# Kernel tuning notes

Hardware: AMD Instinct MI355X
Metric: run time of the kernel (lower is better)

The kernel has to match this reference:

```python
import jax, jax.numpy as jnp
import numpy as np

D = 128      # d_model
H = 8        # nhead
DH = D // H  # head dim
L = 3        # encoder layers
DFF = 2048   # TransformerEncoderLayer default dim_feedforward
S = 1024     # seq_len (number of VRP points)
B = 1        # batch (must be 1: original code's flat-argmax masking)


def setup_inputs() -> dict:
    key = jax.random.key(0)
    ks = jax.random.split(key, 16)
    def w(k, shape, fan_in):
        return jax.random.normal(k, shape, jnp.float32) * (1.0 / np.sqrt(fan_in))
    inp = {}
    inp['x'] = jax.random.normal(ks[0], (B, S, 2), jnp.float32)
    inp['emb_w'] = w(ks[1], (D, 2), 2); inp['emb_b'] = jnp.zeros((D,), jnp.float32)
    inp['in_proj_w'] = w(ks[2], (L, 3 * D, D), D); inp['in_proj_b'] = jnp.zeros((L, 3 * D), jnp.float32)
    inp['out_w'] = w(ks[3], (L, D, D), D); inp['out_b'] = jnp.zeros((L, D), jnp.float32)
    inp['lin1_w'] = w(ks[4], (L, DFF, D), D); inp['lin1_b'] = jnp.zeros((L, DFF), jnp.float32)
    inp['lin2_w'] = w(ks[5], (L, D, DFF), DFF); inp['lin2_b'] = jnp.zeros((L, D), jnp.float32)
    inp['ln1_g'] = jnp.ones((L, D), jnp.float32); inp['ln1_b'] = jnp.zeros((L, D), jnp.float32)
    inp['ln2_g'] = jnp.ones((L, D), jnp.float32); inp['ln2_b'] = jnp.zeros((L, D), jnp.float32)
    inp['lstm_wih'] = w(ks[6], (4 * D, D), D); inp['lstm_whh'] = w(ks[7], (4 * D, D), D)
    inp['lstm_bih'] = jnp.zeros((4 * D,), jnp.float32); inp['lstm_bhh'] = jnp.zeros((4 * D,), jnp.float32)
    inp['ptr_w1'] = w(ks[8], (D, 2 * D), 2 * D); inp['ptr_b1'] = jnp.zeros((D,), jnp.float32)
    inp['ptr_w2'] = w(ks[9], (1, D), D); inp['ptr_b2'] = jnp.zeros((1,), jnp.float32)
    return inp


def _ln(x, g, b, eps=1e-5):
    mu = jnp.mean(x, axis=-1, keepdims=True)
    v = jnp.mean((x - mu) ** 2, axis=-1, keepdims=True)
    return (x - mu) * jax.lax.rsqrt(v + eps) * g + b


def reference(x, emb_w, emb_b, in_proj_w, in_proj_b, out_w, out_b,
              lin1_w, lin1_b, lin2_w, lin2_b, ln1_g, ln1_b, ln2_g, ln2_b,
              lstm_wih, lstm_whh, lstm_bih, lstm_bhh,
              ptr_w1, ptr_b1, ptr_w2, ptr_b2):
    Bz, Sz, _ = x.shape
    # embedding + seq-first layout (torch: permute(1,0,2)) -> [S, B, D]
    xe = (x @ emb_w.T + emb_b).transpose(1, 0, 2)
    scale = 1.0 / np.sqrt(DH)
    # post-norm TransformerEncoder, eval mode (dropout off)
    for l in range(L):
        qkv = xe @ in_proj_w[l].T + in_proj_b[l]                 # [S,B,3D]
        q, k, v = jnp.split(qkv, 3, axis=-1)
        q = q.reshape(Sz, Bz, H, DH)
        k = k.reshape(Sz, Bz, H, DH)
        v = v.reshape(Sz, Bz, H, DH)
        att = jax.nn.softmax(jnp.einsum('qbhd,kbhd->bhqk', q, k) * scale, axis=-1)
        ao = jnp.einsum('bhqk,kbhd->qbhd', att, v).reshape(Sz, Bz, D)
        ao = ao @ out_w[l].T + out_b[l]
        x1 = _ln(xe + ao, ln1_g[l], ln1_b[l])
        ff = jax.nn.relu(x1 @ lin1_w[l].T + lin1_b[l]) @ lin2_w[l].T + lin2_b[l]
        xe = _ln(x1 + ff, ln2_g[l], ln2_b[l])
    encoded = xe                                                  # [S,B,D]

    def lstm_step(inp, h, c):
        g = inp @ lstm_wih.T + lstm_bih + h @ lstm_whh.T + lstm_bhh
        i, f, gc, o = jnp.split(g, 4, axis=-1)                    # torch gate order i,f,g,o
        c = jax.nn.sigmoid(f) * c + jax.nn.sigmoid(i) * jnp.tanh(gc)
        h = jax.nn.sigmoid(o) * jnp.tanh(c)
        return h, c

    def step(carry, _):
        h, c, dec, mask = carry
        h, c = lstm_step(dec, h, c)                               # [B,D]
        pi = jnp.concatenate([encoded, jnp.broadcast_to(h[None], (Sz, Bz, D))], axis=-1)
        logits = (jax.nn.relu(pi @ ptr_w1.T + ptr_b1) @ ptr_w2.T + ptr_b2)[..., 0]  # [S,B]
        logits = jnp.where(mask, -jnp.inf, logits)
        # torch: mask[out.argmax()] = True -> flat argmax == row index when B==1
        mask = mask.at[jnp.argmax(logits)].set(True)
        idx = jnp.argmax(logits, axis=0)                          # [B]
        dec = jnp.take(encoded, idx, axis=0)[0]                   # torch encoded[idx] -> [1,1,D] for B=1
        return (h, c, dec, mask), logits

    carry0 = (jnp.zeros((Bz, D), x.dtype), jnp.zeros((Bz, D), x.dtype),
              encoded[0], jnp.zeros((Sz, Bz), dtype=bool))
    _, logits_all = jax.lax.scan(step, carry0, None, length=Sz - 1)
    return logits_all                                             # [S-1, S, B]
```

## Files before the change

### kernel.cpp

```cpp
#include <hip/hip_runtime.h>
#include <hip/hip_runtime_api.h>
#include <math.h>

typedef unsigned long long ull;

#define F4(p) (*(const float4*)(p))

#define NEG_BIG (-3.0e38f)

__global__ void k_embed(const float* __restrict__ x, const float* __restrict__ ew,
                        const float* __restrict__ eb, float* __restrict__ xe) {
  int i = blockIdx.x * blockDim.x + threadIdx.x;
  int s = i >> 7, d = i & 127;
  xe[i] = fmaf(x[2 * s], ew[2 * d], fmaf(x[2 * s + 1], ew[2 * d + 1], eb[d]));
}

__global__ __launch_bounds__(256) void k_gemm64(
    const float* __restrict__ A, int lda,
    const float* __restrict__ W, int ldw,
    const float* __restrict__ bias, const float* __restrict__ bias2,
    const float* __restrict__ R, float* __restrict__ C,
    int N, int K, int relu) {
  __shared__ __align__(16) float At[32][72];
  __shared__ __align__(16) float Wt[32][72];
  const int t = threadIdx.x;
  const int bm = blockIdx.x, bn = blockIdx.y;
  const int lr = t >> 3;
  const int lk = (t & 7) * 4;
  const int ty = t >> 4, tx = t & 15;
  float acc[4][4];
#pragma unroll
  for (int i = 0; i < 4; ++i)
#pragma unroll
    for (int j = 0; j < 4; ++j) acc[i][j] = 0.f;

  const float* Ab = A + (bm * 64) * lda;
  const float* Wb = W + (bn * 64) * ldw;
  for (int kt = 0; kt < K; kt += 32) {
    float4 a0 = F4(Ab + lr * lda + kt + lk);
    float4 a1 = F4(Ab + (lr + 32) * lda + kt + lk);
    float4 w0 = F4(Wb + lr * ldw + kt + lk);
    float4 w1 = F4(Wb + (lr + 32) * ldw + kt + lk);
    __syncthreads();
    At[lk + 0][lr] = a0.x; At[lk + 1][lr] = a0.y; At[lk + 2][lr] = a0.z; At[lk + 3][lr] = a0.w;
    At[lk + 0][lr + 32] = a1.x; At[lk + 1][lr + 32] = a1.y; At[lk + 2][lr + 32] = a1.z; At[lk + 3][lr + 32] = a1.w;
    Wt[lk + 0][lr] = w0.x; Wt[lk + 1][lr] = w0.y; Wt[lk + 2][lr] = w0.z; Wt[lk + 3][lr] = w0.w;
    Wt[lk + 0][lr + 32] = w1.x; Wt[lk + 1][lr + 32] = w1.y; Wt[lk + 2][lr + 32] = w1.z; Wt[lk + 3][lr + 32] = w1.w;
    __syncthreads();
#pragma unroll
    for (int kk = 0; kk < 32; ++kk) {
      float4 av = F4(&At[kk][4 * ty]);
      float4 wv = F4(&Wt[kk][4 * tx]);
      acc[0][0] = fmaf(av.x, wv.x, acc[0][0]);
      acc[0][1] = fmaf(av.x, wv.y, acc[0][1]);
      acc[0][2] = fmaf(av.x, wv.z, acc[0][2]);
      acc[0][3] = fmaf(av.x, wv.w, acc[0][3]);
      acc[1][0] = fmaf(av.y, wv.x, acc[1][0]);
      acc[1][1] = fmaf(av.y, wv.y, acc[1][1]);
      acc[1][2] = fmaf(av.y, wv.z, acc[1][2]);
      acc[1][3] = fmaf(av.y, wv.w, acc[1][3]);
      acc[2][0] = fmaf(av.z, wv.x, acc[2][0]);
      acc[2][1] = fmaf(av.z, wv.y, acc[2][1]);
      acc[2][2] = fmaf(av.z, wv.z, acc[2][2]);
      acc[2][3] = fmaf(av.z, wv.w, acc[2][3]);
      acc[3][0] = fmaf(av.w, wv.x, acc[3][0]);
      acc[3][1] = fmaf(av.w, wv.y, acc[3][1]);
      acc[3][2] = fmaf(av.w, wv.z, acc[3][2]);
      acc[3][3] = fmaf(av.w, wv.w, acc[3][3]);
    }
  }
#pragma unroll
  for (int i = 0; i < 4; ++i) {
#pragma unroll
    for (int j = 0; j < 4; ++j) {
      int row = bm * 64 + 4 * ty + i, col = bn * 64 + 4 * tx + j;
      float v = acc[i][j];
      if (bias) v += bias[col];
      if (bias2) v += bias2[col];
      if (R) v += R[row * N + col];
      if (relu) v = fmaxf(v, 0.f);
      C[row * N + col] = v;
    }
  }
}

__global__ __launch_bounds__(256) void k_gemm32(
    const float* __restrict__ A, int lda,
    const float* __restrict__ W, int ldw,
    const float* __restrict__ bias, const float* __restrict__ bias2,
    const float* __restrict__ R, float* __restrict__ C,
    int N, int K, int relu) {
  __shared__ __align__(16) float As[32][33];
  __shared__ __align__(16) float Ws[32][33];
  const int t = threadIdx.x;
  const int bm = blockIdx.x, bn = blockIdx.y;
  const int lr = t >> 3;
  const int lk = (t & 7) * 4;
  const int ty = t >> 4, tx = t & 15;
  float a00 = 0.f, a01 = 0.f, a10 = 0.f, a11 = 0.f;
  const float* Ab = A + (bm * 32) * lda;
  const float* Wb = W + (bn * 32) * ldw;
  for (int kt = 0; kt < K; kt += 32) {
    float4 av = F4(Ab + lr * lda + kt + lk);
    float4 wv = F4(Wb + lr * ldw + kt + lk);
    __syncthreads();
    As[lr][lk + 0] = av.x; As[lr][lk + 1] = av.y; As[lr][lk + 2] = av.z; As[lr][lk + 3] = av.w;
    Ws[lr][lk + 0] = wv.x; Ws[lr][lk + 1] = wv.y; Ws[lr][lk + 2] = wv.z; Ws[lr][lk + 3] = wv.w;
    __syncthreads();
#pragma unroll
    for (int kk = 0; kk < 32; ++kk) {
      float x0 = As[2 * ty][kk], x1 = As[2 * ty + 1][kk];
      float y0 = Ws[2 * tx][kk], y1 = Ws[2 * tx + 1][kk];
      a00 = fmaf(x0, y0, a00);
      a01 = fmaf(x0, y1, a01);
      a10 = fmaf(x1, y0, a10);
      a11 = fmaf(x1, y1, a11);
    }
  }
  float accs[2][2] = {{a00, a01}, {a10, a11}};
#pragma unroll
  for (int i = 0; i < 2; ++i) {
#pragma unroll
    for (int j = 0; j < 2; ++j) {
      int row = bm * 32 + 2 * ty + i, col = bn * 32 + 2 * tx + j;
      float v = accs[i][j];
      if (bias) v += bias[col];
      if (bias2) v += bias2[col];
      if (R) v += R[row * N + col];
      if (relu) v = fmaxf(v, 0.f);
      C[row * N + col] = v;
    }
  }
}

__global__ void k_ln(const float* __restrict__ in, const float* __restrict__ g,
                     const float* __restrict__ bln, float* __restrict__ out) {
  int r = blockIdx.x, t = threadIdx.x;
  float a = in[r * 128 + t], c = in[r * 128 + 64 + t];
  float sum = a + c;
#pragma unroll
  for (int off = 32; off >= 1; off >>= 1) sum += __shfl_xor(sum, off);
  float mu = sum * 0.0078125f;
  float da = a - mu, dc = c - mu;
  float v = fmaf(da, da, dc * dc);
#pragma unroll
  for (int off = 32; off >= 1; off >>= 1) v += __shfl_xor(v, off);
  float rs = rsqrtf(fmaf(v, 0.0078125f, 1e-5f));
  out[r * 128 + t] = fmaf(da * rs, g[t], bln[t]);
  out[r * 128 + 64 + t] = fmaf(dc * rs, g[64 + t], bln[64 + t]);
}

__global__ __launch_bounds__(512) void k_attn(const float* __restrict__ qkv,
                                              float* __restrict__ ao) {
  __shared__ __align__(16) float Kt[16][128];
  __shared__ __align__(16) float Vt[16][128];
  const int h = blockIdx.x, qt = blockIdx.y;
  const int t = threadIdx.x;
  const int ql = t >> 4, part = t & 15;
  const int qrow = qt * 32 + ql;
  float qv[16];
#pragma unroll
  for (int i4 = 0; i4 < 4; ++i4) {
    float4 f = F4(qkv + qrow * 384 + h * 16 + 4 * i4);
    qv[4 * i4 + 0] = f.x; qv[4 * i4 + 1] = f.y; qv[4 * i4 + 2] = f.z; qv[4 * i4 + 3] = f.w;
  }
  float m = -INFINITY, l = 0.f;
  float o[16];
#pragma unroll
  for (int i = 0; i < 16; ++i) o[i] = 0.f;

  const int jl = t >> 2, c4 = (t & 3) * 4;
  for (int jt = 0; jt < 8; ++jt) {
    __syncthreads();
    float4 kf = F4(qkv + (jt * 128 + jl) * 384 + 128 + h * 16 + c4);
    float4 vf = F4(qkv + (jt * 128 + jl) * 384 + 256 + h * 16 + c4);
    Kt[c4 + 0][jl] = kf.x; Kt[c4 + 1][jl] = kf.y; Kt[c4 + 2][jl] = kf.z; Kt[c4 + 3][jl] = kf.w;
    Vt[c4 + 0][jl] = vf.x; Vt[c4 + 1][jl] = vf.y; Vt[c4 + 2][jl] = vf.z; Vt[c4 + 3][jl] = vf.w;
    __syncthreads();
    for (int jj = 0; jj < 8; ++jj) {
      int j2 = jj * 16 + part;
      float sc = 0.f;
#pragma unroll
      for (int i = 0; i < 16; ++i) sc = fmaf(qv[i], Kt[i][j2], sc);
      sc *= 0.25f;
      float mn = fmaxf(m, sc);
      float corr = __expf(m - mn);
      float p = __expf(sc - mn);
      l = fmaf(l, corr, p);
#pragma unroll
      for (int i = 0; i < 16; ++i) o[i] = fmaf(o[i], corr, p * Vt[i][j2]);
      m = mn;
    }
  }
#pragma unroll
  for (int off = 1; off < 16; off <<= 1) {
    float m2 = __shfl_xor(m, off), l2 = __shfl_xor(l, off);
    float M = fmaxf(m, m2);
    float c1 = __expf(m - M), c2 = __expf(m2 - M);
    l = l * c1 + l2 * c2;
#pragma unroll
    for (int i = 0; i < 16; ++i) {
      float o2 = __shfl_xor(o[i], off);
      o[i] = o[i] * c1 + o2 * c2;
    }
    m = M;
  }
  if (part == 0) {
    float inv = 1.f / l;
#pragma unroll
    for (int i = 0; i < 16; ++i) ao[qrow * 128 + h * 16 + i] = o[i] * inv;
  }
}

__global__ void k_esum(const float* __restrict__ E1, const float* __restrict__ w2,
                       const float* __restrict__ b2, float* __restrict__ Es) {
  int s = blockIdx.x, t = threadIdx.x;
  float p = E1[s * 128 + t] * w2[t] + E1[s * 128 + 64 + t] * w2[64 + t];
#pragma unroll
  for (int off = 32; off >= 1; off >>= 1) p += __shfl_xor(p, off);
  if (t == 0) Es[s] = fmaf(0.5f, p, b2[0]);
}

__global__ void k_zero(ull* slots) {
  int i = blockIdx.x * blockDim.x + threadIdx.x;
  if (i < 4092) slots[i] = 0ULL;
}

#define DEC_LDS_FLOATS 35352
#define DEC_LDS_BYTES (DEC_LDS_FLOATS * 4)

__global__ __launch_bounds__(1024) void k_decoder(
    const float* __restrict__ E1, const float* __restrict__ Esum2,
    const float* __restrict__ G, const float* __restrict__ Whh,
    const float* __restrict__ PW1, const float* __restrict__ w2,
    ull* __restrict__ slots, float* __restrict__ out) {
  extern __shared__ float lds[];
  float* e1t = lds;
  float* hbuf = lds + 32896;
  float* gbuf = hbuf + 128;
  float* ginb = gbuf + 512;
  float* hpb = ginb + 512;
  float* w2hb = hpb + 128;
  float* accb = w2hb + 128;
  float* redv = accb + 1024;
  int* redi = (int*)(redv + 4);
  ull* keyb = (ull*)(redv + 8);
  float* hsumb = (float*)(keyb + 4);

  const int t = threadIdx.x, b = blockIdx.x;
  const int s = t & 255, q = t >> 8;
  const int r = t >> 1, half = t & 1;
  const int dd = t >> 3, oct = t & 7;

  float whh_reg[64];
#pragma unroll
  for (int kk = 0; kk < 16; ++kk) {
    float4 f = F4(Whh + r * 128 + half * 64 + kk * 4);
    whh_reg[4 * kk + 0] = f.x; whh_reg[4 * kk + 1] = f.y;
    whh_reg[4 * kk + 2] = f.z; whh_reg[4 * kk + 3] = f.w;
  }
  float w1_reg[16];
#pragma unroll
  for (int kk = 0; kk < 4; ++kk) {
    float4 f = F4(PW1 + dd * 256 + 128 + oct * 16 + kk * 4);
    w1_reg[4 * kk + 0] = f.x; w1_reg[4 * kk + 1] = f.y;
    w1_reg[4 * kk + 2] = f.z; w1_reg[4 * kk + 3] = f.w;
  }
  float esum_reg = 0.f, maskf = 0.f;
  if (q == 0) esum_reg = Esum2[b * 256 + s];
  float cval = 0.f;
  float curg = 0.f;
  if (t < 512) curg = G[t];

#pragma unroll
  for (int it = 0; it < 8; ++it) {
    int idx = t + it * 1024;
    int srow = idx >> 5, c4 = (idx & 31) * 4;
    float4 f = F4(E1 + (b * 256 + srow) * 128 + c4);
    e1t[(c4 + 0) * 257 + srow] = f.x;
    e1t[(c4 + 1) * 257 + srow] = f.y;
    e1t[(c4 + 2) * 257 + srow] = f.z;
    e1t[(c4 + 3) * 257 + srow] = f.w;
  }
  if (t < 128) {
    w2hb[t] = 0.5f * w2[t];
    hbuf[t] = 0.f;
  }
  __syncthreads();

#pragma unroll 1
  for (int st = 0; st < 1023; ++st) {
    float p = 0.f;
#pragma unroll
    for (int kk = 0; kk < 16; ++kk) {
      float4 hv = F4(hbuf + half * 64 + kk * 4);
      p = fmaf(whh_reg[4 * kk + 0], hv.x, p);
      p = fmaf(whh_reg[4 * kk + 1], hv.y, p);
      p = fmaf(whh_reg[4 * kk + 2], hv.z, p);
      p = fmaf(whh_reg[4 * kk + 3], hv.w, p);
    }
    p += __shfl_xor(p, 1);
    if (half == 0) gbuf[r] = p;
    if (t < 512) ginb[t] = curg;
    __syncthreads();

    if (t < 128) {
      float gi = gbuf[t] + ginb[t];
      float gf = gbuf[128 + t] + ginb[128 + t];
      float gg = gbuf[256 + t] + ginb[256 + t];
      float go = gbuf[384 + t] + ginb[384 + t];
      float si = 1.f / (1.f + expf(-gi));
      float sf = 1.f / (1.f + expf(-gf));
      float so = 1.f / (1.f + expf(-go));
      float tg = tanhf(gg);
      cval = fmaf(sf, cval, si * tg);
      hbuf[t] = so * tanhf(cval);
    }
    __syncthreads();

    float p2 = 0.f;
#pragma unroll
    for (int kk = 0; kk < 4; ++kk) {
      float4 hv = F4(hbuf + oct * 16 + kk * 4);
      p2 = fmaf(w1_reg[4 * kk + 0], hv.x, p2);
      p2 = fmaf(w1_reg[4 * kk + 1], hv.y, p2);
      p2 = fmaf(w1_reg[4 * kk + 2], hv.z, p2);
      p2 = fmaf(w1_reg[4 * kk + 3], hv.w, p2);
    }
    p2 += __shfl_xor(p2, 1);
    p2 += __shfl_xor(p2, 2);
    p2 += __shfl_xor(p2, 4);
    if (oct == 0) hpb[dd] = p2;
    __syncthreads();

    if (t < 64) {
      float hs = hpb[t] * w2hb[t] + hpb[64 + t] * w2hb[64 + t];
#pragma unroll
      for (int off = 32; off >= 1; off >>= 1) hs += __shfl_xor(hs, off);
      if (t == 0) hsumb[0] = hs;
    }
    float acc = 0.f;
    {
      const float* ebase = e1t + (q * 32) * 257 + s;
      const float* hpq = hpb + q * 32;
      const float* w2q = w2hb + q * 32;
#pragma unroll
      for (int c = 0; c < 8; ++c) {
        float4 hp4 = F4(hpq + c * 4);
        float4 w4 = F4(w2q + c * 4);
        float e0 = ebase[(c * 4 + 0) * 257];
        float e1v = ebase[(c * 4 + 1) * 257];
        float e2 = ebase[(c * 4 + 2) * 257];
        float e3 = ebase[(c * 4 + 3) * 257];
        float y0 = e0 + hp4.x, y1 = e1v + hp4.y, y2 = e2 + hp4.z, y3 = e3 + hp4.w;
        acc = fmaf(w4.x, fabsf(y0), acc);
        acc = fmaf(w4.y, fabsf(y1), acc);
        acc = fmaf(w4.z, fabsf(y2), acc);
        acc = fmaf(w4.w, fabsf(y3), acc);
      }
    }
    accb[q * 256 + s] = acc;
    __syncthreads();

    if (t < 256) {
      float a = accb[t] + accb[256 + t] + accb[512 + t] + accb[768 + t];
      float logit = esum_reg + hsumb[0] + a;
      if (maskf != 0.f) logit = NEG_BIG;
      out[st * 1024 + b * 256 + t] = logit;
      float bv = logit;
      int bi = t;
#pragma unroll
      for (int off = 32; off >= 1; off >>= 1) {
        float ov = __shfl_down(bv, off);
        int oi = __shfl_down(bi, off);
        if (ov > bv || (ov == bv && oi < bi)) { bv = ov; bi = oi; }
      }
      if ((t & 63) == 0) { redv[t >> 6] = bv; redi[t >> 6] = bi; }
    }
    __syncthreads();

    if (t == 0) {
      float bv = redv[0];
      int bi = redi[0];
      for (int w = 1; w < 4; ++w) {
        float ov = redv[w];
        int oi = redi[w];
        if (ov > bv || (ov == bv && oi < bi)) { bv = ov; bi = oi; }
      }
      unsigned u = __float_as_uint(bv);
      u = (u & 0x80000000u) ? ~u : (u | 0x80000000u);
      ull key = (1ULL << 60) | ((ull)u << 12) | (ull)(1023 - (b * 256 + bi));
      __hip_atomic_store(&slots[st * 4 + b], key, __ATOMIC_RELEASE,
                         __HIP_MEMORY_SCOPE_AGENT);
    }
    if (t < 4) {
      ull k;
      do {
        k = __hip_atomic_load(&slots[st * 4 + t], __ATOMIC_ACQUIRE,
                              __HIP_MEMORY_SCOPE_AGENT);
      } while (k == 0ULL);
      keyb[t] = k;
    }
    __syncthreads();

    ull bk = keyb[0];
    if (keyb[1] > bk) bk = keyb[1];
    if (keyb[2] > bk) bk = keyb[2];
    if (keyb[3] > bk) bk = keyb[3];
    int gidx = 1023 - (int)(bk & 0xFFFull);
    if (q == 0 && (b * 256 + s) == gidx) maskf = 1.f;
    if (t < 512) curg = G[gidx * 512 + t];
  }
}

extern "C" void kernel_launch(void* const* d_in, const int* in_sizes, int n_in,
                              void* d_out, int out_size, void* d_ws, size_t ws_size,
                              hipStream_t stream) {
  (void)in_sizes; (void)n_in; (void)out_size; (void)ws_size;
  const float* x = (const float*)d_in[0];
  const float* emb_w = (const float*)d_in[1];
  const float* emb_b = (const float*)d_in[2];
  const float* in_proj_w = (const float*)d_in[3];
  const float* in_proj_b = (const float*)d_in[4];
  const float* out_w = (const float*)d_in[5];
  const float* out_b = (const float*)d_in[6];
  const float* lin1_w = (const float*)d_in[7];
  const float* lin1_b = (const float*)d_in[8];
  const float* lin2_w = (const float*)d_in[9];
  const float* lin2_b = (const float*)d_in[10];
  const float* ln1_g = (const float*)d_in[11];
  const float* ln1_b = (const float*)d_in[12];
  const float* ln2_g = (const float*)d_in[13];
  const float* ln2_b = (const float*)d_in[14];
  const float* lstm_wih = (const float*)d_in[15];
  const float* lstm_whh = (const float*)d_in[16];
  const float* lstm_bih = (const float*)d_in[17];
  const float* lstm_bhh = (const float*)d_in[18];
  const float* ptr_w1 = (const float*)d_in[19];
  const float* ptr_b1 = (const float*)d_in[20];
  const float* ptr_w2 = (const float*)d_in[21];
  const float* ptr_b2 = (const float*)d_in[22];

  float* ws = (float*)d_ws;
  float* xe = ws + 0;
  float* x1 = ws + 131072;
  float* tmp = ws + 262144;
  float* ao = ws + 393216;
  float* qkv = ws + 524288;
  float* ff = ws + 917504;
  float* Gb = ws + 3014656;
  float* E1b = ws + 3538944;
  float* Esb = ws + 3670016;
  ull* slots = (ull*)(ws + 3671040);

  hipFuncSetAttribute((const void*)k_decoder,
                      hipFuncAttributeMaxDynamicSharedMemorySize, DEC_LDS_BYTES);

  k_embed<<<256, 512, 0, stream>>>(x, emb_w, emb_b, xe);
  for (int l = 0; l < 3; ++l) {
    k_gemm64<<<dim3(16, 6), 256, 0, stream>>>(xe, 128, in_proj_w + l * 384 * 128, 128,
        in_proj_b + l * 384, nullptr, nullptr, qkv, 384, 128, 0);
    k_attn<<<dim3(8, 32), 512, 0, stream>>>(qkv, ao);
    k_gemm32<<<dim3(32, 4), 256, 0, stream>>>(ao, 128, out_w + l * 128 * 128, 128,
        out_b + l * 128, nullptr, xe, tmp, 128, 128, 0);
    k_ln<<<1024, 64, 0, stream>>>(tmp, ln1_g + l * 128, ln1_b + l * 128, x1);
    k_gemm64<<<dim3(16, 32), 256, 0, stream>>>(x1, 128, lin1_w + l * 2048 * 128, 128,
        lin1_b + l * 2048, nullptr, nullptr, ff, 2048, 128, 1);
    k_gemm32<<<dim3(32, 4), 256, 0, stream>>>(ff, 2048, lin2_w + l * 128 * 2048, 2048,
        lin2_b + l * 128, nullptr, x1, tmp, 128, 2048, 0);
    k_ln<<<1024, 64, 0, stream>>>(tmp, ln2_g + l * 128, ln2_b + l * 128, xe);
  }
  k_gemm64<<<dim3(16, 8), 256, 0, stream>>>(xe, 128, lstm_wih, 128, lstm_bih, lstm_bhh,
      nullptr, Gb, 512, 128, 0);
  k_gemm32<<<dim3(32, 4), 256, 0, stream>>>(xe, 128, ptr_w1, 256, ptr_b1, nullptr,
      nullptr, E1b, 128, 128, 0);
  k_esum<<<1024, 64, 0, stream>>>(E1b, ptr_w2, ptr_b2, Esb);
  k_zero<<<16, 256, 0, stream>>>(slots);
  k_decoder<<<4, 1024, DEC_LDS_BYTES, stream>>>(E1b, Esb, Gb, lstm_whh, ptr_w1, ptr_w2,
      slots, (float*)d_out);
}
```

Measured before the change: 7.476 ms.

## Collapse decoder argmax and cross-block exchange into one wavefront with atomic max

Moves the per-step argmax into a single wavefront that builds packed value/index keys and reduces them with shuffles. Each block then publishes its key with an atomic fetch_max and polls all four slots inside the same wave, which removes one block-wide barrier and the serial thread-0 merge. Logit stores go to other waves in parallel, and the next step's input-gate row is fetched by wave 0 straight into LDS. Relaxed atomics replace release/acquire, which relies on the loop's barriers and atomics for correct ordering. Adds a launch bound hint and a larger LDS allocation.

Result: faster. 7.013 ms (-6.2%).

```diff
diff --git a/kernel.cpp b/kernel.cpp
--- a/kernel.cpp
+++ b/kernel.cpp
@@ -226,10 +226,10 @@
   if (i < 4092) slots[i] = 0ULL;
 }
 
-#define DEC_LDS_FLOATS 35352
+#define DEC_LDS_FLOATS 35840
 #define DEC_LDS_BYTES (DEC_LDS_FLOATS * 4)
 
-__global__ __launch_bounds__(1024) void k_decoder(
+__global__ __launch_bounds__(1024, 4) void k_decoder(
     const float* __restrict__ E1, const float* __restrict__ Esum2,
     const float* __restrict__ G, const float* __restrict__ Whh,
     const float* __restrict__ PW1, const float* __restrict__ w2,
@@ -241,16 +241,15 @@
   float* ginb = gbuf + 512;
   float* hpb = ginb + 512;
   float* w2hb = hpb + 128;
-  float* accb = w2hb + 128;
-  float* redv = accb + 1024;
-  int* redi = (int*)(redv + 4);
-  ull* keyb = (ull*)(redv + 8);
-  float* hsumb = (float*)(keyb + 4);
+  float* esumb = w2hb + 128;
+  float* maskb = esumb + 256;
+  float* accb = maskb + 256;
 
   const int t = threadIdx.x, b = blockIdx.x;
   const int s = t & 255, q = t >> 8;
   const int r = t >> 1, half = t & 1;
   const int dd = t >> 3, oct = t & 7;
+  const int L = t & 63, wv = t >> 6;
 
   float whh_reg[64];
 #pragma unroll
@@ -266,11 +265,7 @@
     w1_reg[4 * kk + 0] = f.x; w1_reg[4 * kk + 1] = f.y;
     w1_reg[4 * kk + 2] = f.z; w1_reg[4 * kk + 3] = f.w;
   }
-  float esum_reg = 0.f, maskf = 0.f;
-  if (q == 0) esum_reg = Esum2[b * 256 + s];
   float cval = 0.f;
-  float curg = 0.f;
-  if (t < 512) curg = G[t];
 
 #pragma unroll
   for (int it = 0; it < 8; ++it) {
@@ -282,11 +277,12 @@
     e1t[(c4 + 2) * 257 + srow] = f.z;
     e1t[(c4 + 3) * 257 + srow] = f.w;
   }
-  if (t < 128) {
-    w2hb[t] = 0.5f * w2[t];
-    hbuf[t] = 0.f;
-  }
+  if (t < 128) { w2hb[t] = 0.5f * w2[t]; hbuf[t] = 0.f; }
+  if (t < 256) { esumb[t] = Esum2[b * 256 + t]; maskb[t] = 0.f; }
+  if (t < 512) ginb[t] = G[t];
   __syncthreads();
+
+  int gidx = 0;
 
 #pragma unroll 1
   for (int st = 0; st < 1023; ++st) {
@@ -301,7 +297,6 @@
     }
     p += __shfl_xor(p, 1);
     if (half == 0) gbuf[r] = p;
-    if (t < 512) ginb[t] = curg;
     __syncthreads();
 
     if (t < 128) {
@@ -333,12 +328,6 @@
     if (oct == 0) hpb[dd] = p2;
     __syncthreads();
 
-    if (t < 64) {
-      float hs = hpb[t] * w2hb[t] + hpb[64 + t] * w2hb[64 + t];
-#pragma unroll
-      for (int off = 32; off >= 1; off >>= 1) hs += __shfl_xor(hs, off);
-      if (t == 0) hsumb[0] = hs;
-    }
     float acc = 0.f;
     {
       const float* ebase = e1t + (q * 32) * 257 + s;
@@ -362,54 +351,66 @@
     accb[q * 256 + s] = acc;
     __syncthreads();
 
-    if (t < 256) {
-      float a = accb[t] + accb[256 + t] + accb[512 + t] + accb[768 + t];
-      float logit = esum_reg + hsumb[0] + a;
-      if (maskf != 0.f) logit = NEG_BIG;
-      out[st * 1024 + b * 256 + t] = logit;
-      float bv = logit;
-      int bi = t;
-#pragma unroll
-      for (int off = 32; off >= 1; off >>= 1) {
-        float ov = __shfl_down(bv, off);
-        int oi = __shfl_down(bi, off);
-        if (ov > bv || (ov == bv && oi < bi)) { bv = ov; bi = oi; }
-      }
-      if ((t & 63) == 0) { redv[t >> 6] = bv; redi[t >> 6] = bi; }
-    }
-    __syncthreads();
-
-    if (t == 0) {
-      float bv = redv[0];
-      int bi = redi[0];
-      for (int w = 1; w < 4; ++w) {
-        float ov = redv[w];
-        int oi = redi[w];
-        if (ov > bv || (ov == bv && oi < bi)) { bv = ov; bi = oi; }
-      }
-      unsigned u = __float_as_uint(bv);
-      u = (u & 0x80000000u) ? ~u : (u | 0x80000000u);
-      ull key = (1ULL << 60) | ((ull)u << 12) | (ull)(1023 - (b * 256 + bi));
-      __hip_atomic_store(&slots[st * 4 + b], key, __ATOMIC_RELEASE,
-                         __HIP_MEMORY_SCOPE_AGENT);
-    }
-    if (t < 4) {
-      ull k;
-      do {
-        k = __hip_atomic_load(&slots[st * 4 + t], __ATOMIC_ACQUIRE,
-                              __HIP_MEMORY_SCOPE_AGENT);
-      } while (k == 0ULL);
-      keyb[t] = k;
-    }
-    __syncthreads();
-
-    ull bk = keyb[0];
-    if (keyb[1] > bk) bk = keyb[1];
-    if (keyb[2] > bk) bk = keyb[2];
-    if (keyb[3] > bk) bk = keyb[3];
-    int gidx = 1023 - (int)(bk & 0xFFFull);
-    if (q == 0 && (b * 256 + s) == gidx) maskf = 1.f;
-    if (t < 512) curg = G[gidx * 512 + t];
+    if (wv == 0) {
+      float hs = hpb[L] * w2hb[L] + hpb[64 + L] * w2hb[64 + L];
+#pragma unroll
+      for (int off = 32; off >= 1; off >>= 1) hs += __shfl_xor(hs, off);
+      ull bk = 0;
+#pragma unroll
+      for (int j = 0; j < 4; ++j) {
+        int rr = L + 64 * j;
+        float a = (accb[rr] + accb[256 + rr]) + (accb[512 + rr] + accb[768 + rr]);
+        float lg = esumb[rr] + hs + a;
+        if (maskb[rr] != 0.f) lg = NEG_BIG;
+        unsigned u = __float_as_uint(lg);
+        u = (u & 0x80000000u) ? ~u : (u | 0x80000000u);
+        ull key = ((ull)u << 12) | (ull)(1023 - (b * 256 + rr));
+        if (key > bk) bk = key;
+      }
+#pragma unroll
+      for (int off = 1; off < 64; off <<= 1) {
+        ull o = __shfl_xor(bk, off);
+        if (o > bk) bk = o;
+      }
+      if (t == 0)
+        __hip_atomic_fetch_max(&slots[st * 4 + b], bk | (1ULL << 60),
+                               __ATOMIC_RELAXED, __HIP_MEMORY_SCOPE_AGENT);
+      ull k = 0;
+      if (L < 4) {
+        do {
+          k = __hip_atomic_fetch_or(&slots[st * 4 + L], 0ULL,
+                                    __ATOMIC_RELAXED, __HIP_MEMORY_SCOPE_AGENT);
+        } while (k == 0ULL);
+      }
+#pragma unroll
+      for (int off = 1; off < 64; off <<= 1) {
+        ull o = __shfl_xor(k, off);
+        if (o > k) k = o;
+      }
+      gidx = 1023 - (int)(k & 0x3FFull);
+    } else if (wv >= 4 && wv < 8) {
+      float hs = hpb[L] * w2hb[L] + hpb[64 + L] * w2hb[64 + L];
+#pragma unroll
+      for (int off = 32; off >= 1; off >>= 1) hs += __shfl_xor(hs, off);
+      int rr = t - 256;
+      float a = (accb[rr] + accb[256 + rr]) + (accb[512 + rr] + accb[768 + rr]);
+      float lg = esumb[rr] + hs + a;
+      if (maskb[rr] != 0.f) lg = NEG_BIG;
+      out[st * 1024 + b * 256 + rr] = lg;
+    }
+    __syncthreads();
+
+    if (wv == 0) {
+      if (t == 0) {
+        int loc = gidx - b * 256;
+        if ((unsigned)loc < 256u) maskb[loc] = 1.f;
+      }
+      const float* gsrc = G + (size_t)gidx * 512 + L * 8;
+      float4 g0 = F4(gsrc);
+      float4 g1 = F4(gsrc + 4);
+      *(float4*)(ginb + L * 8) = g0;
+      *(float4*)(ginb + L * 8 + 4) = g1;
+    }
   }
 }
 
```
